# Kernel optimization log

Hardware: AMD Instinct MI355X
Metric: run time of the kernel (lower is better)

## Reference

```python
import jax, jax.numpy as jnp
import numpy as np

EPS = 1e-12


def pairwise_sqdist(x, y):
    # x: (B, N, 3), y: (B, M, 3) -> (B, N, M) squared euclidean distances
    xx = jnp.sum(x * x, axis=-1)              # (B, N)
    yy = jnp.sum(y * y, axis=-1)              # (B, M)
    xy = jnp.einsum('bnd,bmd->bnm', x, y)     # (B, N, M)
    d = xx[:, :, None] + yy[None_ if False else yy[:, None, :].shape and 0 or ...] if False else xx[:, :, None] + yy[:, None, :] - 2.0 * xy
    return jnp.maximum(d, 0.0)


def chamfer_l1(x, y):
    # pytorch3d/PoinTr-style ChamferDistanceL1:
    # mean over points of sqrt(min squared dist), averaged over both directions
    d = pairwise_sqdist(x, y)                 # (B, N, M)
    d1 = jnp.min(d, axis=2)                   # (B, N) x -> nearest y
    d2 = jnp.min(d, axis=1)                   # (B, M) y -> nearest x
    d1 = jnp.sqrt(jnp.maximum(d1, EPS))
    d2 = jnp.sqrt(jnp.maximum(d2, EPS))
    return 0.5 * (jnp.mean(d1) + jnp.mean(d2))


def knn1_gather(x, y):
    # For each point in x (B,N,3), find nearest neighbor in y (B,M,3) (K=1)
    # and gather it -> (B, N, 3). Matches knn_points + knn_gather + squeeze.
    d = pairwise_sqdist(x, y)                 # (B, N, M)
    idx = jnp.argmin(d, axis=2)               # (B, N) int
    return jnp.take_along_axis(y, idx[:, :, None], axis=1)  # (B, N, 3)


def volume_with_wedge(p):
    # wedge-product volume over consecutive point triples:
    # V = sum_i (p_i x p_{i+1}) . p_{i+2} / 6  -> (B,)
    c = jnp.cross(p[:, :-2, :], p[:, 1:-1, :])  # (B, N-2, 3)
    return jnp.sum(jnp.einsum('bnd,bnd->bn', c, p[:, 2:, :]), axis=-1) / 6.0


def setup_inputs() -> dict:
    key = jax.random.key(0)
    k1, k2, k3 = jax.random.split(key, 3)
    B, Nc, Nf, M = 2, 512, 8192, 8192
    return {
        'source_coarse': jax.random.normal(k1, (B, Nc, 3), dtype=jnp.float32),
        'source_fine': jax.random.normal(k2, (B, Nf, 3), dtype=jnp.float32),
        'target_points': jax.random.normal(k3, (B, M, 3), dtype=jnp.float32),
    }


def reference(source_coarse, source_fine, target_points):
    lambda_rot = lambda_ref = lambda_align = lambda_geo = 1.0
    B = source_fine.shape[0]
    axis = jnp.broadcast_to(jnp.array([0.0, 0.0, 1.0], dtype=source_fine.dtype), (B, 3))
    plane_normal = jnp.broadcast_to(jnp.array([0.0, 1.0, 0.0], dtype=source_fine.dtype), (B, 3))

    # KNN (K=1) gather of nearest target point for each fine source point
    new_target = knn1_gather(source_fine, target_points)  # (B, Nf, 3)

    # alignment (Chamfer L1) losses
    loss_align_coarse = chamfer_l1(source_coarse, target_points)
    loss_align_fine = chamfer_l1(source_fine, target_points)

    # rotational symmetry loss
    in_proj = jnp.einsum('bij,bj->bi', source_fine, axis)      # (B, Nf)
    re_proj = jnp.einsum('bij,bj->bi', new_target, axis)
    loss_rot = jnp.mean((jnp.linalg.norm(in_proj, axis=-1) - jnp.linalg.norm(re_proj, axis=-1)) ** 2)

    # reflectional symmetry loss
    pn = plane_normal / jnp.linalg.norm(plane_normal, axis=-1, keepdims=True)
    in_dist = jnp.einsum('bij,bj->bi', source_fine, pn)
    re_dist = jnp.einsum('bij,bj->bi', new_target, pn)
    loss_ref = jnp.mean((in_dist - re_dist) ** 2)

    # geometric consistency (wedge-product volume) loss
    loss_geo = jnp.mean((volume_with_wedge(source_fine) - volume_with_wedge(new_target)) ** 2)

    total = (lambda_rot * loss_rot + lambda_ref * loss_ref
             + lambda_align * loss_align_coarse + lambda_align * loss_align_fine
             + lambda_geo * loss_geo)
    return total
```

## Files before the change

kernel.cpp:

```cpp
#include <hip/hip_runtime.h>
#include <stdint.h>
#include <float.h>

using u64 = unsigned long long;
typedef float v2f __attribute__((ext_vector_type(2)));

constexpr int B_ = 2;
constexpr int NC = 512;
constexpr int NF = 8192;
constexpr int MT = 8192;

constexpr int TPB = 256;
constexpr int CFF = 32;
constexpr int CCR = 128;
constexpr int CCC = 8;
constexpr int TAIL_BLOCKS = 196;

#define DEVINL __device__ __forceinline__

template<bool ARGMIN, int R2t, int NJ>
DEVINL void pairmin_phase(const float* __restrict__ P, const float* __restrict__ Q,
                          int nP, int nQ, int b, int row_base, int j0,
                          int chunk, int nRowsTot,
                          u64* __restrict__ outPack, unsigned* __restrict__ outVal,
                          float4* tile)
{
#pragma clang fp contract(off)
    const int tid = threadIdx.x;

    v2f tx0[R2t], tx1[R2t], tx2[R2t], txx[R2t], dbest[R2t];
    int jb[2 * R2t];
    #pragma unroll
    for (int r = 0; r < R2t; ++r) {
        const int row0 = row_base + tid + (2 * r) * TPB;
        const int row1 = row_base + tid + (2 * r + 1) * TPB;
        const float* p0 = P + ((size_t)b * nP + row0) * 3;
        const float* p1 = P + ((size_t)b * nP + row1) * 3;
        float a0 = p0[0], a1 = p0[1], a2 = p0[2];
        float e0 = p1[0], e1 = p1[1], e2 = p1[2];
        tx0[r] = v2f{2.0f * a0, 2.0f * e0};
        tx1[r] = v2f{2.0f * a1, 2.0f * e1};
        tx2[r] = v2f{2.0f * a2, 2.0f * e2};
        txx[r] = v2f{(a0*a0 + a1*a1) + a2*a2, (e0*e0 + e1*e1) + e2*e2};
        dbest[r] = v2f{FLT_MAX, FLT_MAX};
        jb[2 * r] = 0; jb[2 * r + 1] = 0;
    }

    __syncthreads();
    if (tid < NJ) {
        const float* q = Q + ((size_t)b * nQ + j0 + tid) * 3;
        float q0 = q[0], q1 = q[1], q2 = q[2];
        tile[tid] = make_float4(q0, q1, q2, (q0*q0 + q1*q1) + q2*q2);
    }
    __syncthreads();

    auto PROC = [&](const float4 qv, const int j) {
#pragma clang fp contract(off)
        #pragma unroll
        for (int r = 0; r < R2t; ++r) {
            v2f s = (tx0[r] * qv.x + tx1[r] * qv.y) + tx2[r] * qv.z;
            v2f d = (txx[r] + qv.w) - s;
            if (ARGMIN) {
                bool c0 = d.x < dbest[r].x;
                bool c1 = d.y < dbest[r].y;
                dbest[r].x = c0 ? d.x : dbest[r].x;
                dbest[r].y = c1 ? d.y : dbest[r].y;
                jb[2 * r]     = c0 ? j : jb[2 * r];
                jb[2 * r + 1] = c1 ? j : jb[2 * r + 1];
            } else {
                dbest[r] = __builtin_elementwise_min(dbest[r], d);
            }
        }
    };

    float4 qa[4], qb[4];
    #pragma unroll
    for (int u = 0; u < 4; ++u) qa[u] = tile[u];
    for (int jj = 0; jj < NJ; jj += 8) {
        #pragma unroll
        for (int u = 0; u < 4; ++u) qb[u] = tile[jj + 4 + u];
        #pragma unroll
        for (int u = 0; u < 4; ++u) PROC(qa[u], j0 + jj + u);
        #pragma unroll
        for (int u = 0; u < 4; ++u) qa[u] = tile[(jj + 8 + u) & (NJ - 1)];
        #pragma unroll
        for (int u = 0; u < 4; ++u) PROC(qb[u], j0 + jj + 4 + u);
    }

    const v2f vzero = {0.0f, 0.0f};
    const size_t o0 = (size_t)chunk * nRowsTot + (size_t)b * nP;
    #pragma unroll
    for (int r = 0; r < R2t; ++r) {
        v2f dcl = __builtin_elementwise_max(dbest[r], vzero);
        const int row0 = row_base + tid + (2 * r) * TPB;
        const int row1 = row_base + tid + (2 * r + 1) * TPB;
        if (ARGMIN) {
            outPack[o0 + row0] = ((u64)__float_as_uint(dcl.x) << 32) | (unsigned)jb[2 * r];
            outPack[o0 + row1] = ((u64)__float_as_uint(dcl.y) << 32) | (unsigned)jb[2 * r + 1];
        } else {
            outVal[o0 + row0] = __float_as_uint(dcl.x);
            outVal[o0 + row1] = __float_as_uint(dcl.y);
        }
    }
}

__global__ __launch_bounds__(TPB, 2) void pairmin_all(
    const float* __restrict__ coarse, const float* __restrict__ fine,
    const float* __restrict__ tgt,
    u64* __restrict__ pfr, unsigned* __restrict__ pfc,
    unsigned* __restrict__ pcr, unsigned* __restrict__ pcc,
    unsigned* __restrict__ counter)
{
    __shared__ float4 tile[256];
    const int bx = blockIdx.x;
    if (bx == 0 && threadIdx.x == 0) *counter = 0;
    if (bx < 256) {
        const int b = bx >> 7, g = (bx >> 5) & 3, c = bx & 31;
        pairmin_phase<true, 4, 256>(fine, tgt, NF, MT, b, g * 2048, c * 256,
                                    c, B_ * NF, pfr, nullptr, tile);
        pairmin_phase<false, 1, 64>(coarse, tgt, NC, MT, bx >> 7, 0, (bx & 127) * 64,
                                    bx & 127, B_ * NC, nullptr, pcr, tile);
    } else {
        const int i = bx - 256;
        const int b = i >> 7, g = (i >> 5) & 3, c = i & 31;
        pairmin_phase<false, 4, 256>(tgt, fine, MT, NF, b, g * 2048, c * 256,
                                     c, B_ * MT, nullptr, pfc, tile);
        pairmin_phase<false, 1, 64>(tgt, coarse, MT, NC, i >> 7, ((i >> 3) & 15) * 512,
                                    (i & 7) * 64, i & 7, B_ * MT, nullptr, pcc, tile);
    }
}

__global__ __launch_bounds__(TPB) void tail_all(
    const float* __restrict__ fine, const float* __restrict__ tgt,
    const u64* __restrict__ pfr, const unsigned* __restrict__ pfc,
    const unsigned* __restrict__ pcr, const unsigned* __restrict__ pcc,
    double* __restrict__ bs, unsigned* __restrict__ counter,
    float* __restrict__ out)
{
    __shared__ float sp[TPB + 2][3], yp[TPB + 2][3];
    __shared__ double redw[4][9];
    __shared__ double lred[4][13];
    __shared__ int lastflag;
    const int bx = blockIdx.x, tid = threadIdx.x;
    const int wave = tid >> 6, lane = tid & 63;

    double v_s = 0, v_d2f = 0, v_d1c = 0, v_d2c = 0, v_yd2 = 0, v_zs = 0, v_zt = 0;
    double vs = 0, vt = 0;
    int role_b = 0;

    if (bx < 64) {
        const int base = bx * TPB;
        const int g = base + tid;
        const int b = base >> 13;  role_b = b;
        u64 best = pfr[g];
        #pragma unroll
        for (int cc = 1; cc < CFF; ++cc) {
            u64 p = pfr[(size_t)cc * (B_ * NF) + g];
            best = p < best ? p : best;
        }
        float d1 = __uint_as_float((unsigned)(best >> 32));
        int idx  = (int)(best & 0xffffffffULL);
        float s = sqrtf(fmaxf(d1, 1e-12f));
        const float* y  = tgt  + ((size_t)b * MT + idx) * 3;
        const float* sr = fine + (size_t)g * 3;
        float y0 = y[0],  y1 = y[1],  y2 = y[2];
        float s0 = sr[0], s1 = sr[1], s2 = sr[2];
        yp[tid][0] = y0; yp[tid][1] = y1; yp[tid][2] = y2;
        sp[tid][0] = s0; sp[tid][1] = s1; sp[tid][2] = s2;
        const int base_b = base & (NF - 1);
        if (tid < 2 && base_b + TPB + tid < NF) {
            int g2 = base + TPB + tid;
            u64 b2 = pfr[g2];
            #pragma unroll
            for (int cc = 1; cc < CFF; ++cc) {
                u64 p = pfr[(size_t)cc * (B_ * NF) + g2];
                b2 = p < b2 ? p : b2;
            }
            int i2 = (int)(b2 & 0xffffffffULL);
            const float* yh = tgt  + ((size_t)b * MT + i2) * 3;
            const float* sh = fine + (size_t)g2 * 3;
            #pragma unroll
            for (int k = 0; k < 3; ++k) { yp[TPB + tid][k] = yh[k]; sp[TPB + tid][k] = sh[k]; }
        }
        __syncthreads();
        v_s = s;
        float yd = s1 - y1;
        v_yd2 = (double)(yd * yd);
        v_zs  = (double)(s2 * s2);
        v_zt  = (double)(y2 * y2);
        int rb = base_b + tid;
        if (rb <= NF - 3) {
            {
                const float* a = sp[tid]; const float* c2 = sp[tid+1]; const float* e = sp[tid+2];
                float c0 = a[1]*c2[2] - a[2]*c2[1];
                float c1 = a[2]*c2[0] - a[0]*c2[2];
                float c2v = a[0]*c2[1] - a[1]*c2[0];
                vs = (double)(c0*e[0] + c1*e[1] + c2v*e[2]);
            }
            {
                const float* a = yp[tid]; const float* c2 = yp[tid+1]; const float* e = yp[tid+2];
                float c0 = a[1]*c2[2] - a[2]*c2[1];
                float c1 = a[2]*c2[0] - a[0]*c2[2];
                float c2v = a[0]*c2[1] - a[1]*c2[0];
                vt = (double)(c0*e[0] + c1*e[1] + c2v*e[2]);
            }
        }
    } else if (bx < 128) {
        const int g = (bx - 64) * TPB + tid;
        unsigned best = pfc[g];
        #pragma unroll
        for (int cc = 1; cc < CFF; ++cc) best = min(best, pfc[(size_t)cc * (B_ * MT) + g]);
        v_d2f = (double)sqrtf(fmaxf(__uint_as_float(best), 1e-12f));
    } else if (bx < 132) {
        const int g = (bx - 128) * TPB + tid;
        unsigned best = pcr[g];
        #pragma unroll 16
        for (int cc = 1; cc < CCR; ++cc) best = min(best, pcr[(size_t)cc * (B_ * NC) + g]);
        v_d1c = (double)sqrtf(fmaxf(__uint_as_float(best), 1e-12f));
    } else {
        const int g = (bx - 132) * TPB + tid;
        unsigned best = pcc[g];
        #pragma unroll
        for (int cc = 1; cc < CCC; ++cc) best = min(best, pcc[(size_t)cc * (B_ * MT) + g]);
        v_d2c = (double)sqrtf(fmaxf(__uint_as_float(best), 1e-12f));
    }

    double r9[9] = {v_s, v_d2f, v_d1c, v_d2c, v_yd2, v_zs, v_zt, vs, vt};
    for (int o = 32; o; o >>= 1) {
        #pragma unroll
        for (int k = 0; k < 9; ++k) r9[k] += __shfl_down(r9[k], o);
    }
    if (lane == 0) {
        #pragma unroll
        for (int k = 0; k < 9; ++k) redw[wave][k] = r9[k];
    }
    __syncthreads();
    if (tid == 0) {
        double t9[9];
        #pragma unroll
        for (int k = 0; k < 9; ++k)
            t9[k] = redw[0][k] + redw[1][k] + redw[2][k] + redw[3][k];
        double* o = bs + (size_t)bx * 16;
        #pragma unroll
        for (int k = 0; k < 16; ++k) o[k] = 0.0;
        o[0] = t9[0]; o[1] = t9[1]; o[2] = t9[2]; o[3] = t9[3]; o[4] = t9[4];
        o[5 + role_b]  = t9[5];
        o[7 + role_b]  = t9[6];
        o[9 + role_b]  = t9[7];
        o[11 + role_b] = t9[8];
        __threadfence();
        unsigned old = atomicAdd(counter, 1u);
        lastflag = (old == TAIL_BLOCKS - 1);
    }
    __syncthreads();
    if (!lastflag) return;

    __threadfence();
    double c13[13];
    if (tid < TAIL_BLOCKS) {
        const double* p = bs + (size_t)tid * 16;
        #pragma unroll
        for (int k = 0; k < 13; ++k) c13[k] = p[k];
    } else {
        #pragma unroll
        for (int k = 0; k < 13; ++k) c13[k] = 0.0;
    }
    for (int o = 32; o; o >>= 1) {
        #pragma unroll
        for (int k = 0; k < 13; ++k) c13[k] += __shfl_down(c13[k], o);
    }
    if (lane == 0) {
        #pragma unroll
        for (int k = 0; k < 13; ++k) lred[wave][k] = c13[k];
    }
    __syncthreads();
    if (tid == 0) {
        double S[13];
        #pragma unroll
        for (int k = 0; k < 13; ++k)
            S[k] = lred[0][k] + lred[1][k] + lred[2][k] + lred[3][k];
        double m_d1f = S[0] / (double)(B_ * NF);
        double m_d2f = S[1] / (double)(B_ * MT);
        double m_d1c = S[2] / (double)(B_ * NC);
        double m_d2c = S[3] / (double)(B_ * MT);
        double loss_align_fine   = 0.5 * (m_d1f + m_d2f);
        double loss_align_coarse = 0.5 * (m_d1c + m_d2c);
        double loss_ref = S[4] / (double)(B_ * NF);
        double loss_rot = 0.0, loss_geo = 0.0;
        for (int b = 0; b < B_; ++b) {
            double dn = sqrt(S[5 + b]) - sqrt(S[7 + b]);
            loss_rot += dn * dn;
            double dv = (S[9 + b] - S[11 + b]) / 6.0;
            loss_geo += dv * dv;
        }
        loss_rot /= (double)B_;
        loss_geo /= (double)B_;
        out[0] = (float)(loss_rot + loss_ref + loss_align_coarse + loss_align_fine + loss_geo);
    }
}

extern "C" void kernel_launch(void* const* d_in, const int* in_sizes, int n_in,
                              void* d_out, int out_size, void* d_ws, size_t ws_size,
                              hipStream_t stream)
{
    const float* src_coarse = (const float*)d_in[0];
    const float* src_fine   = (const float*)d_in[1];
    const float* tgt        = (const float*)d_in[2];
    float* out = (float*)d_out;
    char*  ws  = (char*)d_ws;

    u64*      pfr     = (u64*)(ws);
    unsigned* pfc     = (unsigned*)(ws + 4194304);
    unsigned* pcr     = (unsigned*)(ws + 6291456);
    unsigned* pcc     = (unsigned*)(ws + 6815744);
    double*   bs      = (double*)(ws + 7340032);
    unsigned* counter = (unsigned*)(ws + 7365120);

    pairmin_all<<<dim3(512), TPB, 0, stream>>>(
        src_coarse, src_fine, tgt, pfr, pfc, pcr, pcc, counter);
    tail_all<<<dim3(TAIL_BLOCKS), TPB, 0, stream>>>(
        src_fine, tgt, pfr, pfc, pcr, pcc, bs, counter, out);
}
```

Before: 120.3 us.

## Fuse pairmin and tail kernels with grid-wide atomic barrier and rebalance fine work split

Merges the two kernels into one launch: all 512 blocks compute partial minima, then signal an atomic done counter, and the first 196 blocks spin-wait on it before running the reduction tail. The fine-vs-target work is now split so every block does both directions over 128-column chunks (64 chunks instead of 32), which balances per-block load but doubles the partial-result buffers the tail must reduce. This removes one kernel launch gap at the cost of a memset launch and a spin barrier that depends on all 512 blocks being co-resident.

After: 202.7 us. +68.4%, slower.

```diff
diff --git a/kernel.cpp b/kernel.cpp
--- a/kernel.cpp
+++ b/kernel.cpp
@@ -10,10 +10,11 @@
 constexpr int NF = 8192;
 constexpr int MT = 8192;
 
-constexpr int TPB = 256;
-constexpr int CFF = 32;
-constexpr int CCR = 128;
-constexpr int CCC = 8;
+constexpr int TPB  = 256;
+constexpr int NBLK = 512;
+constexpr int CFF  = 64;
+constexpr int CCR  = 128;
+constexpr int CCC  = 8;
 constexpr int TAIL_BLOCKS = 196;
 
 #define DEVINL __device__ __forceinline__
@@ -104,39 +105,15 @@
     }
 }
 
-__global__ __launch_bounds__(TPB, 2) void pairmin_all(
+__global__ __launch_bounds__(TPB, 2) void fused_all(
     const float* __restrict__ coarse, const float* __restrict__ fine,
     const float* __restrict__ tgt,
     u64* __restrict__ pfr, unsigned* __restrict__ pfc,
     unsigned* __restrict__ pcr, unsigned* __restrict__ pcc,
-    unsigned* __restrict__ counter)
+    double* __restrict__ bs, unsigned* __restrict__ done,
+    unsigned* __restrict__ counter, float* __restrict__ out)
 {
-    __shared__ float4 tile[256];
-    const int bx = blockIdx.x;
-    if (bx == 0 && threadIdx.x == 0) *counter = 0;
-    if (bx < 256) {
-        const int b = bx >> 7, g = (bx >> 5) & 3, c = bx & 31;
-        pairmin_phase<true, 4, 256>(fine, tgt, NF, MT, b, g * 2048, c * 256,
-                                    c, B_ * NF, pfr, nullptr, tile);
-        pairmin_phase<false, 1, 64>(coarse, tgt, NC, MT, bx >> 7, 0, (bx & 127) * 64,
-                                    bx & 127, B_ * NC, nullptr, pcr, tile);
-    } else {
-        const int i = bx - 256;
-        const int b = i >> 7, g = (i >> 5) & 3, c = i & 31;
-        pairmin_phase<false, 4, 256>(tgt, fine, MT, NF, b, g * 2048, c * 256,
-                                     c, B_ * MT, nullptr, pfc, tile);
-        pairmin_phase<false, 1, 64>(tgt, coarse, MT, NC, i >> 7, ((i >> 3) & 15) * 512,
-                                    (i & 7) * 64, i & 7, B_ * MT, nullptr, pcc, tile);
-    }
-}
-
-__global__ __launch_bounds__(TPB) void tail_all(
-    const float* __restrict__ fine, const float* __restrict__ tgt,
-    const u64* __restrict__ pfr, const unsigned* __restrict__ pfc,
-    const unsigned* __restrict__ pcr, const unsigned* __restrict__ pcc,
-    double* __restrict__ bs, unsigned* __restrict__ counter,
-    float* __restrict__ out)
-{
+    __shared__ float4 tile[128];
     __shared__ float sp[TPB + 2][3], yp[TPB + 2][3];
     __shared__ double redw[4][9];
     __shared__ double lred[4][13];
@@ -144,6 +121,35 @@
     const int bx = blockIdx.x, tid = threadIdx.x;
     const int wave = tid >> 6, lane = tid & 63;
 
+    {
+        const int b  = bx >> 8;
+        const int rg = (bx >> 6) & 3;
+        const int jc = bx & 63;
+        pairmin_phase<true, 4, 128>(fine, tgt, NF, MT, b, rg * 2048, jc * 128,
+                                    jc, B_ * NF, pfr, nullptr, tile);
+        pairmin_phase<false, 4, 128>(tgt, fine, MT, NF, b, rg * 2048, jc * 128,
+                                     jc, B_ * MT, nullptr, pfc, tile);
+        if (bx < 256) {
+            pairmin_phase<false, 1, 64>(coarse, tgt, NC, MT, bx >> 7, 0, (bx & 127) * 64,
+                                        bx & 127, B_ * NC, nullptr, pcr, tile);
+        } else {
+            const int i = bx - 256;
+            pairmin_phase<false, 1, 64>(tgt, coarse, MT, NC, i >> 7, ((i >> 3) & 15) * 512,
+                                        (i & 7) * 64, i & 7, B_ * MT, nullptr, pcc, tile);
+        }
+    }
+
+    __threadfence();
+    __syncthreads();
+    if (tid == 0)
+        __hip_atomic_fetch_add(done, 1u, __ATOMIC_RELEASE, __HIP_MEMORY_SCOPE_AGENT);
+    if (bx >= TAIL_BLOCKS) return;
+    if (tid == 0) {
+        while (__hip_atomic_load(done, __ATOMIC_ACQUIRE, __HIP_MEMORY_SCOPE_AGENT) < NBLK)
+            __builtin_amdgcn_s_sleep(2);
+    }
+    __syncthreads();
+
     double v_s = 0, v_d2f = 0, v_d1c = 0, v_d2c = 0, v_yd2 = 0, v_zs = 0, v_zt = 0;
     double vs = 0, vt = 0;
     int role_b = 0;
@@ -153,7 +159,7 @@
         const int g = base + tid;
         const int b = base >> 13;  role_b = b;
         u64 best = pfr[g];
-        #pragma unroll
+        #pragma unroll 16
         for (int cc = 1; cc < CFF; ++cc) {
             u64 p = pfr[(size_t)cc * (B_ * NF) + g];
             best = p < best ? p : best;
@@ -171,7 +177,7 @@
         if (tid < 2 && base_b + TPB + tid < NF) {
             int g2 = base + TPB + tid;
             u64 b2 = pfr[g2];
-            #pragma unroll
+            #pragma unroll 16
             for (int cc = 1; cc < CFF; ++cc) {
                 u64 p = pfr[(size_t)cc * (B_ * NF) + g2];
                 b2 = p < b2 ? p : b2;
@@ -208,7 +214,7 @@
     } else if (bx < 128) {
         const int g = (bx - 64) * TPB + tid;
         unsigned best = pfc[g];
-        #pragma unroll
+        #pragma unroll 16
         for (int cc = 1; cc < CFF; ++cc) best = min(best, pfc[(size_t)cc * (B_ * MT) + g]);
         v_d2f = (double)sqrtf(fmaxf(__uint_as_float(best), 1e-12f));
     } else if (bx < 132) {
@@ -310,14 +316,14 @@
     char*  ws  = (char*)d_ws;
 
     u64*      pfr     = (u64*)(ws);
-    unsigned* pfc     = (unsigned*)(ws + 4194304);
-    unsigned* pcr     = (unsigned*)(ws + 6291456);
-    unsigned* pcc     = (unsigned*)(ws + 6815744);
-    double*   bs      = (double*)(ws + 7340032);
-    unsigned* counter = (unsigned*)(ws + 7365120);
-
-    pairmin_all<<<dim3(512), TPB, 0, stream>>>(
-        src_coarse, src_fine, tgt, pfr, pfc, pcr, pcc, counter);
-    tail_all<<<dim3(TAIL_BLOCKS), TPB, 0, stream>>>(
-        src_fine, tgt, pfr, pfc, pcr, pcc, bs, counter, out);
+    unsigned* pfc     = (unsigned*)(ws + 8388608);
+    unsigned* pcr     = (unsigned*)(ws + 12582912);
+    unsigned* pcc     = (unsigned*)(ws + 13107200);
+    double*   bs      = (double*)(ws + 13631488);
+    unsigned* done    = (unsigned*)(ws + 13656576);
+    unsigned* counter = done + 1;
+
+    hipMemsetAsync(done, 0, 8, stream);
+    fused_all<<<dim3(NBLK), TPB, 0, stream>>>(
+        src_coarse, src_fine, tgt, pfr, pfc, pcr, pcc, bs, done, counter, out);
 }
```

## Retile fine pairmin to 8 rows per thread and rebalance coarse work

Applied to the files above, without the earlier changes.

Each fine-pass block now covers 4096 rows by 128 columns, with 8 row-pairs per thread instead of 4, so every loaded target tile is reused across more rows. The column split doubles to 64 chunks, which doubles the partial-result buffers and the tail reduction length. Block roles are interleaved by parity, and both coarse passes now run in the odd blocks, rebalancing work between the two block types. The cost is higher register pressure per thread and more partial-min traffic in the tail kernel.

Result: slower. 131.3 us (+9.1%).

```diff
diff --git a/kernel.cpp b/kernel.cpp
--- a/kernel.cpp
+++ b/kernel.cpp
@@ -11,7 +11,7 @@
 constexpr int MT = 8192;
 
 constexpr int TPB = 256;
-constexpr int CFF = 32;
+constexpr int CFF = 64;
 constexpr int CCR = 128;
 constexpr int CCC = 8;
 constexpr int TAIL_BLOCKS = 196;
@@ -111,22 +111,25 @@
     unsigned* __restrict__ pcr, unsigned* __restrict__ pcc,
     unsigned* __restrict__ counter)
 {
-    __shared__ float4 tile[256];
+    __shared__ float4 tile[128];
     const int bx = blockIdx.x;
     if (bx == 0 && threadIdx.x == 0) *counter = 0;
-    if (bx < 256) {
-        const int b = bx >> 7, g = (bx >> 5) & 3, c = bx & 31;
-        pairmin_phase<true, 4, 256>(fine, tgt, NF, MT, b, g * 2048, c * 256,
-                                    c, B_ * NF, pfr, nullptr, tile);
-        pairmin_phase<false, 1, 64>(coarse, tgt, NC, MT, bx >> 7, 0, (bx & 127) * 64,
-                                    bx & 127, B_ * NC, nullptr, pcr, tile);
+    const int type = bx & 1;
+    const int idx  = bx >> 1;
+    const int b    = idx >> 7;
+    const int slab = (idx >> 6) & 1;
+    const int jc   = idx & 63;
+
+    if (type == 0) {
+        pairmin_phase<true, 8, 128>(fine, tgt, NF, MT, b, slab * 4096, jc * 128,
+                                    jc, B_ * NF, pfr, nullptr, tile);
     } else {
-        const int i = bx - 256;
-        const int b = i >> 7, g = (i >> 5) & 3, c = i & 31;
-        pairmin_phase<false, 4, 256>(tgt, fine, MT, NF, b, g * 2048, c * 256,
-                                     c, B_ * MT, nullptr, pfc, tile);
-        pairmin_phase<false, 1, 64>(tgt, coarse, MT, NC, i >> 7, ((i >> 3) & 15) * 512,
-                                    (i & 7) * 64, i & 7, B_ * MT, nullptr, pcc, tile);
+        pairmin_phase<false, 8, 128>(tgt, fine, MT, NF, b, slab * 4096, jc * 128,
+                                     jc, B_ * MT, nullptr, pfc, tile);
+        pairmin_phase<false, 1, 64>(coarse, tgt, NC, MT, idx >> 7, 0, (idx & 127) * 64,
+                                    idx & 127, B_ * NC, nullptr, pcr, tile);
+        pairmin_phase<false, 1, 64>(tgt, coarse, MT, NC, idx >> 7, ((idx >> 3) & 15) * 512,
+                                    (idx & 7) * 64, idx & 7, B_ * MT, nullptr, pcc, tile);
     }
 }
 
@@ -153,7 +156,7 @@
         const int g = base + tid;
         const int b = base >> 13;  role_b = b;
         u64 best = pfr[g];
-        #pragma unroll
+        #pragma unroll 16
         for (int cc = 1; cc < CFF; ++cc) {
             u64 p = pfr[(size_t)cc * (B_ * NF) + g];
             best = p < best ? p : best;
@@ -171,7 +174,7 @@
         if (tid < 2 && base_b + TPB + tid < NF) {
             int g2 = base + TPB + tid;
             u64 b2 = pfr[g2];
-            #pragma unroll
+            #pragma unroll 16
             for (int cc = 1; cc < CFF; ++cc) {
                 u64 p = pfr[(size_t)cc * (B_ * NF) + g2];
                 b2 = p < b2 ? p : b2;
@@ -208,7 +211,7 @@
     } else if (bx < 128) {
         const int g = (bx - 64) * TPB + tid;
         unsigned best = pfc[g];
-        #pragma unroll
+        #pragma unroll 16
         for (int cc = 1; cc < CFF; ++cc) best = min(best, pfc[(size_t)cc * (B_ * MT) + g]);
         v_d2f = (double)sqrtf(fmaxf(__uint_as_float(best), 1e-12f));
     } else if (bx < 132) {
@@ -310,11 +313,11 @@
     char*  ws  = (char*)d_ws;
 
     u64*      pfr     = (u64*)(ws);
-    unsigned* pfc     = (unsigned*)(ws + 4194304);
-    unsigned* pcr     = (unsigned*)(ws + 6291456);
-    unsigned* pcc     = (unsigned*)(ws + 6815744);
-    double*   bs      = (double*)(ws + 7340032);
-    unsigned* counter = (unsigned*)(ws + 7365120);
+    unsigned* pfc     = (unsigned*)(ws + 8388608);
+    unsigned* pcr     = (unsigned*)(ws + 12582912);
+    unsigned* pcc     = (unsigned*)(ws + 13107200);
+    double*   bs      = (double*)(ws + 13631488);
+    unsigned* counter = (unsigned*)(ws + 13656576);
 
     pairmin_all<<<dim3(512), TPB, 0, stream>>>(
         src_coarse, src_fine, tgt, pfr, pfc, pcr, pcc, counter);
```
